# Kernel optimization log

Measured on AMD Instinct MI355X. Metric: run time of the kernel, lower is better.

Reference implementation:

```python
import jax, jax.numpy as jnp
import numpy as np

# 8 directional difference stencils (N, S, E, W, NE, SE, SW, NW), OIHW [8,1,3,3]
_WINDOWS = np.array([
    [[0, 1, 0], [0, -1, 0], [0, 0, 0]],
    [[0, 0, 0], [0, -1, 0], [0, 1, 0]],
    [[0, 0, 0], [0, -1, 1], [0, 0, 0]],
    [[0, 0, 0], [1, -1, 0], [0, 0, 0]],
    [[0, 0, 1], [0, -1, 0], [0, 0, 0]],
    [[0, 0, 0], [0, -1, 0], [0, 0, 1]],
    [[0, 0, 0], [0, -1, 0], [1, 0, 0]],
    [[1, 0, 0], [0, -1, 0], [0, 0, 0]],
], dtype=np.float32).reshape(8, 1, 3, 3)

ITERATIONS = 30  # int(self.iterations.item()) with init value 30.0


def setup_inputs() -> dict:
    key = jax.random.key(0)
    k1, k2, k3 = jax.random.split(key, 3)
    x = jax.random.normal(k1, (32, 3, 512, 512), dtype=jnp.float32)
    W_expand = jax.random.normal(k2, (3, 3, 1, 1), dtype=jnp.float32) * 0.3
    b_expand = jax.random.normal(k3, (3,), dtype=jnp.float32) * 0.1
    return {
        "x": x,
        "delta": jnp.float32(0.1),
        "kappa": jnp.float32(15.0),
        "W_expand": W_expand,
        "b_expand": b_expand,
    }


def reference(x, delta, kappa, W_expand, b_expand):
    K = jnp.asarray(_WINDOWS)  # [8,1,3,3]
    # axial directions weight 1, diagonal directions weight 1/(sqrt(2))^2 = 0.5
    dir_w = jnp.array([1.0, 1.0, 1.0, 1.0, 0.5, 0.5, 0.5, 0.5],
                      dtype=x.dtype).reshape(1, 8, 1, 1)

    # RGB -> luminance, [B,1,H,W]
    u = (0.299 * x[:, 0] + 0.587 * x[:, 1] + 0.114 * x[:, 2])[:, None]

    def step(u, _):
        # all 8 directional gradients in one grouped conv: [B,8,H,W]
        nabla = jax.lax.conv_general_dilated(
            u, K, window_strides=(1, 1), padding='SAME',
            dimension_numbers=('NCHW', 'OIHW', 'NCHW'))
        diff = 1.0 / (1.0 + (nabla / kappa) ** 2)  # Perona-Malik diffusivity
        upd = jnp.sum(dir_w * diff * nabla, axis=1, keepdims=True)
        return u + delta * upd, None

    u, _ = jax.lax.scan(step, u, None, length=ITERATIONS)

    # repeat to 3 channels then 1x1 conv (expand_channels)
    u_rgb = jnp.repeat(u, 3, axis=1)  # [B,3,H,W]
    out = jnp.einsum('oi,bihw->bohw', W_expand[:, :, 0, 0], u_rgb)
    out = out + b_expand[None, :, None, None]
    return out
```

## Files before the change

### kernel.cpp

```cpp
#include <hip/hip_runtime.h>

#define BATCH 32
#define HGT 512
#define WID 512
#define PLANE (HGT * WID)
#define NPIX (BATCH * PLANE)
#define BSTRIDE (3 * PLANE)
#define WQ (WID / 4)
#define NQUAD (NPIX / 4)

#define RSLAB 16
#define SLABS (HGT / RSLAB)
#define FBLOCKS (BATCH * SLABS)
#define FT 512

__device__ __forceinline__ float4 ld4(const float* p) {
    return *reinterpret_cast<const float4*>(p);
}
__device__ __forceinline__ void st4(float* p, float4 v) {
    *reinterpret_cast<float4*>(p) = v;
}

__device__ __forceinline__ float pm_flux(float d, float ik2) {
    return d * __builtin_amdgcn_rcpf(fmaf(d * d, ik2, 1.f));
}

__device__ __forceinline__ void lds_row6(const float* __restrict__ buf, int row, int quad,
                                         float r[6]) {
    const float* p = buf + row * WID + (quad << 2);
    float4 v = ld4(p);
    r[1] = v.x; r[2] = v.y; r[3] = v.z; r[4] = v.w;
    r[0] = (quad > 0) ? p[-1] : 0.f;
    r[5] = (quad < WQ - 1) ? p[4] : 0.f;
}

__device__ __forceinline__ void level_flux(const float a[6], const float b[6],
                                           float vF[4], float seF[5], float swF[5],
                                           float ik2) {
#pragma unroll
    for (int j = 0; j < 4; ++j) vF[j] = pm_flux(b[j + 1] - a[j + 1], ik2);
#pragma unroll
    for (int i = 0; i < 5; ++i) seF[i] = pm_flux(b[i + 1] - a[i], ik2);
#pragma unroll
    for (int i = 0; i < 5; ++i) swF[i] = pm_flux(b[i] - a[i + 1], ik2);
}

__device__ __forceinline__ void srange(int L0, int L1, int strip, int& s0, int& n) {
    int tot = L1 - L0;
    int base = tot >> 2, rem = tot & 3;
    n = base + (strip < rem ? 1 : 0);
    s0 = L0 + strip * base + (strip < rem ? strip : rem);
}

template <int MODE, int S>
__global__ __launch_bounds__(FT, 4)
void pm_fusedk(const float* __restrict__ src, int sstr,
               float* __restrict__ dst, int dstr,
               const float* __restrict__ pdelta, const float* __restrict__ pkappa,
               const float* __restrict__ Wexp, const float* __restrict__ bexp) {
    constexpr int LR = RSLAB + 2 * S;
    extern __shared__ float buf[];

    const int img   = blockIdx.x >> 5;
    const int slab  = blockIdx.x & (SLABS - 1);
    const int H0    = slab * RSLAB;
    const int tid   = threadIdx.x;
    const int strip = tid >> 7;
    const int quad  = tid & (WQ - 1);

    const float delta = *pdelta;
    const float kappa = *pkappa;
    const float ik2 = __builtin_amdgcn_rcpf(kappa * kappa);

    const float* sb = src + (size_t)img * sstr;
#pragma unroll
    for (int i = tid; i < LR * WQ; i += FT) {
        int row = i >> 7;
        int q   = i & (WQ - 1);
        int g = H0 - S + row;
        float4 v = make_float4(0.f, 0.f, 0.f, 0.f);
        if ((unsigned)g < (unsigned)HGT) {
            const float* p = sb + g * WID + (q << 2);
            if (MODE == 0) {
                float4 r = ld4(p), gg = ld4(p + PLANE), bb = ld4(p + 2 * PLANE);
                v.x = fmaf(0.299f, r.x, fmaf(0.587f, gg.x, 0.114f * bb.x));
                v.y = fmaf(0.299f, r.y, fmaf(0.587f, gg.y, 0.114f * bb.y));
                v.z = fmaf(0.299f, r.z, fmaf(0.587f, gg.z, 0.114f * bb.z));
                v.w = fmaf(0.299f, r.w, fmaf(0.587f, gg.w, 0.114f * bb.w));
            } else {
                v = ld4(p);
            }
        }
        st4(buf + row * WID + (q << 2), v);
    }
    __syncthreads();

    float s0c = 0.f, s1c = 0.f, s2c = 0.f, b0c = 0.f, b1c = 0.f, b2c = 0.f;
    if (MODE == 2) {
        s0c = Wexp[0] + Wexp[1] + Wexp[2];
        s1c = Wexp[3] + Wexp[4] + Wexp[5];
        s2c = Wexp[6] + Wexp[7] + Wexp[8];
        b0c = bexp[0]; b1c = bexp[1]; b2c = bexp[2];
    }

    float* db = dst + (size_t)img * dstr;

#pragma unroll
    for (int s = 0; s < S; ++s) {
        const int L0r = s + 1, L1r = LR - 1 - s;
        int st0, n;
        srange(L0r, L1r, strip, st0, n);

        float4 res[6];
        float a[6], m[6], d6[6];
        lds_row6(buf, st0 - 1, quad, a);
        lds_row6(buf, st0, quad, m);
        float pV[4], pSE[5], pSW[5];
        level_flux(a, m, pV, pSE, pSW, ik2);

#pragma unroll
        for (int i = 0; i < 6; ++i) {
            if (i < n) {
                lds_row6(buf, st0 + i + 1, quad, d6);
                float hF[5];
#pragma unroll
                for (int t = 0; t < 5; ++t) hF[t] = pm_flux(m[t + 1] - m[t], ik2);
                float cV[4], cSE[5], cSW[5];
                level_flux(m, d6, cV, cSE, cSW, ik2);
                float o[4];
#pragma unroll
                for (int j = 0; j < 4; ++j) {
                    float axial = cV[j] - pV[j] + hF[j + 1] - hF[j];
                    float diag  = cSE[j + 1] + cSW[j] - pSE[j] - pSW[j + 1];
                    o[j] = fmaf(delta, fmaf(0.5f, diag, axial), m[j + 1]);
                }
                int g = H0 - S + st0 + i;
                bool in = (unsigned)g < (unsigned)HGT;
                res[i] = in ? make_float4(o[0], o[1], o[2], o[3])
                            : make_float4(0.f, 0.f, 0.f, 0.f);
#pragma unroll
                for (int t = 0; t < 6; ++t) m[t] = d6[t];
#pragma unroll
                for (int j = 0; j < 4; ++j) pV[j] = cV[j];
#pragma unroll
                for (int t = 0; t < 5; ++t) { pSE[t] = cSE[t]; pSW[t] = cSW[t]; }
            }
        }

        if (s == S - 1) {
#pragma unroll
            for (int i = 0; i < 6; ++i) {
                if (i < n) {
                    int g = H0 - S + st0 + i;
                    float* p = db + g * WID + (quad << 2);
                    if (MODE == 2) {
                        float4 u = res[i];
                        st4(p, make_float4(fmaf(s0c, u.x, b0c), fmaf(s0c, u.y, b0c),
                                           fmaf(s0c, u.z, b0c), fmaf(s0c, u.w, b0c)));
                        st4(p + PLANE,
                            make_float4(fmaf(s1c, u.x, b1c), fmaf(s1c, u.y, b1c),
                                        fmaf(s1c, u.z, b1c), fmaf(s1c, u.w, b1c)));
                        st4(p + 2 * PLANE,
                            make_float4(fmaf(s2c, u.x, b2c), fmaf(s2c, u.y, b2c),
                                        fmaf(s2c, u.z, b2c), fmaf(s2c, u.w, b2c)));
                    } else {
                        st4(p, res[i]);
                    }
                }
            }
        } else {
            __syncthreads();
#pragma unroll
            for (int i = 0; i < 6; ++i)
                if (i < n) st4(buf + (st0 + i) * WID + (quad << 2), res[i]);
            __syncthreads();
        }
    }
}

__global__ void expand_from(const float* __restrict__ usrc, int ustr,
                            float* __restrict__ out,
                            const float* __restrict__ Wexp,
                            const float* __restrict__ bexp) {
    int idx = blockIdx.x * blockDim.x + threadIdx.x;
    if (idx >= NQUAD) return;
    int b = idx / (PLANE / 4);
    int off = (idx - b * (PLANE / 4)) * 4;

    float4 u = ld4(usrc + (size_t)b * ustr + off);
    float s0 = Wexp[0] + Wexp[1] + Wexp[2];
    float s1 = Wexp[3] + Wexp[4] + Wexp[5];
    float s2 = Wexp[6] + Wexp[7] + Wexp[8];
    float b0 = bexp[0], b1 = bexp[1], b2 = bexp[2];

    size_t base = (size_t)b * BSTRIDE + off;
    st4(out + base, make_float4(fmaf(s0, u.x, b0), fmaf(s0, u.y, b0),
                                fmaf(s0, u.z, b0), fmaf(s0, u.w, b0)));
    st4(out + base + PLANE, make_float4(fmaf(s1, u.x, b1), fmaf(s1, u.y, b1),
                                        fmaf(s1, u.z, b1), fmaf(s1, u.w, b1)));
    st4(out + base + 2 * PLANE, make_float4(fmaf(s2, u.x, b2), fmaf(s2, u.y, b2),
                                            fmaf(s2, u.z, b2), fmaf(s2, u.w, b2)));
}

extern "C" void kernel_launch(void* const* d_in, const int* in_sizes, int n_in,
                              void* d_out, int out_size, void* d_ws, size_t ws_size,
                              hipStream_t stream) {
    const float* x      = (const float*)d_in[0];
    const float* pdelta = (const float*)d_in[1];
    const float* pkappa = (const float*)d_in[2];
    const float* Wexp   = (const float*)d_in[3];
    const float* bexp   = (const float*)d_in[4];
    float* out = (float*)d_out;

    const int LDS4 = (RSLAB + 8) * WID * 4;
    const int LDS2 = (RSLAB + 4) * WID * 4;

    const size_t need = (size_t)2 * NPIX * sizeof(float);
    if (ws_size >= need) {
        float* uA = (float*)d_ws;
        float* uB = uA + NPIX;
        pm_fusedk<0, 4><<<FBLOCKS, FT, LDS4, stream>>>(
            x, BSTRIDE, uA, PLANE, pdelta, pkappa, Wexp, bexp);
        float* s = uA;
        float* d = uB;
        for (int k = 0; k < 6; ++k) {
            pm_fusedk<1, 4><<<FBLOCKS, FT, LDS4, stream>>>(
                s, PLANE, d, PLANE, pdelta, pkappa, Wexp, bexp);
            float* t = s; s = d; d = t;
        }
        pm_fusedk<2, 2><<<FBLOCKS, FT, LDS2, stream>>>(
            s, PLANE, out, BSTRIDE, pdelta, pkappa, Wexp, bexp);
    } else {
        float* uA = out;
        float* uB = out + PLANE;
        pm_fusedk<0, 4><<<FBLOCKS, FT, LDS4, stream>>>(
            x, BSTRIDE, uA, BSTRIDE, pdelta, pkappa, Wexp, bexp);
        float* s = uA;
        float* d = uB;
        for (int k = 0; k < 6; ++k) {
            pm_fusedk<1, 4><<<FBLOCKS, FT, LDS4, stream>>>(
                s, BSTRIDE, d, BSTRIDE, pdelta, pkappa, Wexp, bexp);
            float* t = s; s = d; d = t;
        }
        pm_fusedk<1, 2><<<FBLOCKS, FT, LDS2, stream>>>(
            s, BSTRIDE, d, BSTRIDE, pdelta, pkappa, Wexp, bexp);
        const int block = 256;
        const int grid_q = (NQUAD + block - 1) / block;
        expand_from<<<grid_q, block, 0, stream>>>(d, BSTRIDE, out, Wexp, bexp);
    }
}
```

Before: 375.9 us.

## Widen fused stencil slabs to 64 rows with wavefront-per-row-pair and in-place interior writes

Raises the slab height from 16 to 64 rows and the block size from 512 to 1024 threads, which cuts the fraction of redundant halo rows recomputed across fused iterations. Each wavefront now covers a full row as two float4 halves and gets its left and right neighbours through cross-lane shuffles instead of extra scalar LDS loads. Interior rows of each strip are written back to LDS as soon as they are computed, and only the first and last row of each strip are held in registers until the barrier. This lowers register pressure and LDS traffic but reduces the number of blocks, which may hurt occupancy or load balance.

```diff
diff --git a/kernel.cpp b/kernel.cpp
--- a/kernel.cpp
+++ b/kernel.cpp
@@ -6,13 +6,13 @@
 #define PLANE (HGT * WID)
 #define NPIX (BATCH * PLANE)
 #define BSTRIDE (3 * PLANE)
-#define WQ (WID / 4)
 #define NQUAD (NPIX / 4)
 
-#define RSLAB 16
+#define RSLAB 64
 #define SLABS (HGT / RSLAB)
 #define FBLOCKS (BATCH * SLABS)
-#define FT 512
+#define FT 1024
+#define MAXN 5
 
 __device__ __forceinline__ float4 ld4(const float* p) {
     return *reinterpret_cast<const float4*>(p);
@@ -23,15 +23,6 @@
 
 __device__ __forceinline__ float pm_flux(float d, float ik2) {
     return d * __builtin_amdgcn_rcpf(fmaf(d * d, ik2, 1.f));
-}
-
-__device__ __forceinline__ void lds_row6(const float* __restrict__ buf, int row, int quad,
-                                         float r[6]) {
-    const float* p = buf + row * WID + (quad << 2);
-    float4 v = ld4(p);
-    r[1] = v.x; r[2] = v.y; r[3] = v.z; r[4] = v.w;
-    r[0] = (quad > 0) ? p[-1] : 0.f;
-    r[5] = (quad < WQ - 1) ? p[4] : 0.f;
 }
 
 __device__ __forceinline__ void level_flux(const float a[6], const float b[6],
@@ -45,11 +36,58 @@
     for (int i = 0; i < 5; ++i) swF[i] = pm_flux(b[i] - a[i + 1], ik2);
 }
 
-__device__ __forceinline__ void srange(int L0, int L1, int strip, int& s0, int& n) {
-    int tot = L1 - L0;
-    int base = tot >> 2, rem = tot & 3;
-    n = base + (strip < rem ? 1 : 0);
-    s0 = L0 + strip * base + (strip < rem ? strip : rem);
+__device__ __forceinline__ void load_row2(const float* __restrict__ buf, int row, int o,
+                                          float rA[6], float rB[6]) {
+    const float* p = buf + row * WID + (o << 2);
+    float4 a = ld4(p);
+    float4 b = ld4(p + 256);
+    float aW63 = __shfl(a.w, 63);
+    float bX0  = __shfl(b.x, 0);
+    float lA   = __shfl_up(a.w, 1);
+    float rAr  = __shfl_down(a.x, 1);
+    float lB   = __shfl_up(b.w, 1);
+    float rBr  = __shfl_down(b.x, 1);
+    rA[0] = (o == 0) ? 0.f : lA;
+    rA[1] = a.x; rA[2] = a.y; rA[3] = a.z; rA[4] = a.w;
+    rA[5] = (o == 63) ? bX0 : rAr;
+    rB[0] = (o == 0) ? aW63 : lB;
+    rB[1] = b.x; rB[2] = b.y; rB[3] = b.z; rB[4] = b.w;
+    rB[5] = (o == 63) ? 0.f : rBr;
+}
+
+struct SegState {
+    float m[6];
+    float pV[4], pSE[5], pSW[5];
+};
+
+__device__ __forceinline__ void seg_init(SegState& S_, const float a6[6],
+                                         const float m6[6], float ik2) {
+#pragma unroll
+    for (int t = 0; t < 6; ++t) S_.m[t] = m6[t];
+    level_flux(a6, m6, S_.pV, S_.pSE, S_.pSW, ik2);
+}
+
+__device__ __forceinline__ float4 seg_step(SegState& S_, const float d6[6],
+                                           float delta, float ik2) {
+    float hF[5];
+#pragma unroll
+    for (int t = 0; t < 5; ++t) hF[t] = pm_flux(S_.m[t + 1] - S_.m[t], ik2);
+    float cV[4], cSE[5], cSW[5];
+    level_flux(S_.m, d6, cV, cSE, cSW, ik2);
+    float o[4];
+#pragma unroll
+    for (int j = 0; j < 4; ++j) {
+        float axial = cV[j] - S_.pV[j] + hF[j + 1] - hF[j];
+        float diag  = cSE[j + 1] + cSW[j] - S_.pSE[j] - S_.pSW[j + 1];
+        o[j] = fmaf(delta, fmaf(0.5f, diag, axial), S_.m[j + 1]);
+    }
+#pragma unroll
+    for (int t = 0; t < 6; ++t) S_.m[t] = d6[t];
+#pragma unroll
+    for (int j = 0; j < 4; ++j) S_.pV[j] = cV[j];
+#pragma unroll
+    for (int t = 0; t < 5; ++t) { S_.pSE[t] = cSE[t]; S_.pSW[t] = cSW[t]; }
+    return make_float4(o[0], o[1], o[2], o[3]);
 }
 
 template <int MODE, int S>
@@ -61,12 +99,12 @@
     constexpr int LR = RSLAB + 2 * S;
     extern __shared__ float buf[];
 
-    const int img   = blockIdx.x >> 5;
+    const int img   = blockIdx.x >> 3;
     const int slab  = blockIdx.x & (SLABS - 1);
     const int H0    = slab * RSLAB;
     const int tid   = threadIdx.x;
-    const int strip = tid >> 7;
-    const int quad  = tid & (WQ - 1);
+    const int strip = tid >> 6;
+    const int o     = tid & 63;
 
     const float delta = *pdelta;
     const float kappa = *pkappa;
@@ -74,9 +112,9 @@
 
     const float* sb = src + (size_t)img * sstr;
 #pragma unroll
-    for (int i = tid; i < LR * WQ; i += FT) {
+    for (int i = tid; i < LR * (WID / 4); i += FT) {
         int row = i >> 7;
-        int q   = i & (WQ - 1);
+        int q   = i & 127;
         int g = H0 - S + row;
         float4 v = make_float4(0.f, 0.f, 0.f, 0.f);
         if ((unsigned)g < (unsigned)HGT) {
@@ -107,72 +145,81 @@
 
 #pragma unroll
     for (int s = 0; s < S; ++s) {
-        const int L0r = s + 1, L1r = LR - 1 - s;
-        int st0, n;
-        srange(L0r, L1r, strip, st0, n);
-
-        float4 res[6];
-        float a[6], m[6], d6[6];
-        lds_row6(buf, st0 - 1, quad, a);
-        lds_row6(buf, st0, quad, m);
-        float pV[4], pSE[5], pSW[5];
-        level_flux(a, m, pV, pSE, pSW, ik2);
-
-#pragma unroll
-        for (int i = 0; i < 6; ++i) {
+        const int L0 = s + 1, L1 = LR - 1 - s;
+        const int tot = L1 - L0;
+        const int bse = tot >> 4, rem = tot & 15;
+        const int n   = bse + (strip < rem ? 1 : 0);
+        const int st0 = L0 + strip * bse + (strip < rem ? strip : rem);
+        const bool fin = (s == S - 1);
+
+        SegState SA, SB;
+        {
+            float a6[6], b6[6], mA[6], mB[6];
+            load_row2(buf, st0 - 1, o, a6, b6);
+            load_row2(buf, st0, o, mA, mB);
+            seg_init(SA, a6, mA, ik2);
+            seg_init(SB, b6, mB, ik2);
+        }
+        float4 fA = make_float4(0, 0, 0, 0), fB = fA, lA4 = fA, lB4 = fA;
+
+#pragma unroll
+        for (int i = 0; i < MAXN; ++i) {
             if (i < n) {
-                lds_row6(buf, st0 + i + 1, quad, d6);
-                float hF[5];
-#pragma unroll
-                for (int t = 0; t < 5; ++t) hF[t] = pm_flux(m[t + 1] - m[t], ik2);
-                float cV[4], cSE[5], cSW[5];
-                level_flux(m, d6, cV, cSE, cSW, ik2);
-                float o[4];
-#pragma unroll
-                for (int j = 0; j < 4; ++j) {
-                    float axial = cV[j] - pV[j] + hF[j + 1] - hF[j];
-                    float diag  = cSE[j + 1] + cSW[j] - pSE[j] - pSW[j + 1];
-                    o[j] = fmaf(delta, fmaf(0.5f, diag, axial), m[j + 1]);
+                float dA[6], dB[6];
+                load_row2(buf, st0 + i + 1, o, dA, dB);
+                float4 rA = seg_step(SA, dA, delta, ik2);
+                float4 rB = seg_step(SB, dB, delta, ik2);
+                const int g = H0 - S + st0 + i;
+                if ((unsigned)g >= (unsigned)HGT) {
+                    rA = make_float4(0, 0, 0, 0);
+                    rB = make_float4(0, 0, 0, 0);
                 }
-                int g = H0 - S + st0 + i;
-                bool in = (unsigned)g < (unsigned)HGT;
-                res[i] = in ? make_float4(o[0], o[1], o[2], o[3])
-                            : make_float4(0.f, 0.f, 0.f, 0.f);
-#pragma unroll
-                for (int t = 0; t < 6; ++t) m[t] = d6[t];
-#pragma unroll
-                for (int j = 0; j < 4; ++j) pV[j] = cV[j];
-#pragma unroll
-                for (int t = 0; t < 5; ++t) { pSE[t] = cSE[t]; pSW[t] = cSW[t]; }
-            }
-        }
-
-        if (s == S - 1) {
-#pragma unroll
-            for (int i = 0; i < 6; ++i) {
-                if (i < n) {
-                    int g = H0 - S + st0 + i;
-                    float* p = db + g * WID + (quad << 2);
+                if (fin) {
+                    float* p = db + (size_t)g * WID + (o << 2);
                     if (MODE == 2) {
-                        float4 u = res[i];
-                        st4(p, make_float4(fmaf(s0c, u.x, b0c), fmaf(s0c, u.y, b0c),
-                                           fmaf(s0c, u.z, b0c), fmaf(s0c, u.w, b0c)));
+                        st4(p, make_float4(fmaf(s0c, rA.x, b0c), fmaf(s0c, rA.y, b0c),
+                                           fmaf(s0c, rA.z, b0c), fmaf(s0c, rA.w, b0c)));
+                        st4(p + 256, make_float4(fmaf(s0c, rB.x, b0c), fmaf(s0c, rB.y, b0c),
+                                                 fmaf(s0c, rB.z, b0c), fmaf(s0c, rB.w, b0c)));
                         st4(p + PLANE,
-                            make_float4(fmaf(s1c, u.x, b1c), fmaf(s1c, u.y, b1c),
-                                        fmaf(s1c, u.z, b1c), fmaf(s1c, u.w, b1c)));
+                            make_float4(fmaf(s1c, rA.x, b1c), fmaf(s1c, rA.y, b1c),
+                                        fmaf(s1c, rA.z, b1c), fmaf(s1c, rA.w, b1c)));
+                        st4(p + PLANE + 256,
+                            make_float4(fmaf(s1c, rB.x, b1c), fmaf(s1c, rB.y, b1c),
+                                        fmaf(s1c, rB.z, b1c), fmaf(s1c, rB.w, b1c)));
                         st4(p + 2 * PLANE,
-                            make_float4(fmaf(s2c, u.x, b2c), fmaf(s2c, u.y, b2c),
-                                        fmaf(s2c, u.z, b2c), fmaf(s2c, u.w, b2c)));
+                            make_float4(fmaf(s2c, rA.x, b2c), fmaf(s2c, rA.y, b2c),
+                                        fmaf(s2c, rA.z, b2c), fmaf(s2c, rA.w, b2c)));
+                        st4(p + 2 * PLANE + 256,
+                            make_float4(fmaf(s2c, rB.x, b2c), fmaf(s2c, rB.y, b2c),
+                                        fmaf(s2c, rB.z, b2c), fmaf(s2c, rB.w, b2c)));
                     } else {
-                        st4(p, res[i]);
+                        st4(p, rA);
+                        st4(p + 256, rB);
                     }
+                } else if (i == 0) {
+                    fA = rA; fB = rB;
+                } else if (i == n - 1) {
+                    lA4 = rA; lB4 = rB;
+                } else {
+                    float* p = buf + (st0 + i) * WID + (o << 2);
+                    st4(p, rA);
+                    st4(p + 256, rB);
                 }
             }
-        } else {
+        }
+        if (!fin) {
             __syncthreads();
-#pragma unroll
-            for (int i = 0; i < 6; ++i)
-                if (i < n) st4(buf + (st0 + i) * WID + (quad << 2), res[i]);
+            {
+                float* p = buf + st0 * WID + (o << 2);
+                st4(p, fA);
+                st4(p + 256, fB);
+            }
+            {
+                float* p = buf + (st0 + n - 1) * WID + (o << 2);
+                st4(p, lA4);
+                st4(p + 256, lB4);
+            }
             __syncthreads();
         }
     }
```

Measured after the change: 536.3 us. 1.43x slower.
